# Kernel tuning notes

Hardware: AMD Instinct MI355X
Metric: run time of the kernel (lower is better)

The kernel has to match this reference:

```python
import jax, jax.numpy as jnp
import numpy as np

NUM_CLASSES = 8
SCORE_T = 0.5
IOU_T = 0.5
POSE_HYPS = 10
MAX_DET = 100
B, A = 1, 4096


def _pairwise_iou(bx):
    # bx: (N,4) in (x1,y1,x2,y2); TF-style +1 pixel convention
    x1 = jnp.maximum(bx[:, None, 0], bx[None, :, 0])
    y1 = jnp.maximum(bx[:, None, 1], bx[None, :, 1])
    x2 = jnp.minimum(bx[:, None, 2], bx[None, :, 2])
    y2 = jnp.minimum(bx[:, None, 3], bx[None, :, 3])
    wid = x2 - x1 + 1.0
    hei = y2 - y1 + 1.0
    inter = wid * hei
    area = (bx[:, 2] - bx[:, 0] + 1.0) * (bx[:, 3] - bx[:, 1] + 1.0)
    den = area[:, None] + area[None, :] - inter
    ov = jnp.where(den == 0.0, 0.0, inter / jnp.where(den == 0.0, 1.0, den))  # divide_no_nan
    return jnp.where((wid <= 0.0) | (hei <= 0.0), 0.0, ov)


def _per_class(scores_c, boxes_c, poses_c, conf_c):
    # Fixed-shape re-expression of _filter_detections: instead of compacting the
    # boxes with score > threshold (dynamic shape), keep all N and mask invalid
    # boxes out of the overlap indicator. Relative ordering (which drives the
    # argmax tie-break and the ascending sort) is identical to the compacted
    # subset, so the math matches exactly.
    N = scores_c.shape[0]
    K = POSE_HYPS + 1
    valid = scores_c > SCORE_T
    m = jnp.sum(valid.astype(jnp.int32))  # number of selected boxes
    ov = _pairwise_iou(boxes_c)  # (N,N)
    ind = ((ov > IOU_T) & valid[:, None] & valid[None, :]).astype(jnp.float32)
    # scatter_nd: true_ov[argmax_col(row i), i] = max(row i); column i is unique per update
    max_col = jnp.argmax(ind, axis=1)
    true_ov = jnp.zeros_like(ind).at[max_col, jnp.arange(N)].add(jnp.max(ind, axis=1))
    bc = (1.0 - ov) * true_ov * conf_c[None, :]
    bc = jnp.where(bc == 0.0, 1000.0, bc)  # 1000 = sentinel for 'not a hypothesis'
    # Only the first min(pose_hyps+1, m) ascending-sorted entries per row survive the
    # sequence mask, so take the K smallest instead of a full argsort (same result;
    # top_k of the negation breaks ties by lowest index like a stable ascending sort).
    neg, args = jax.lax.top_k(-bc, K)
    svals = -neg  # (N,K) K smallest per row
    hyp = (jnp.arange(K) < jnp.minimum(K, m)).astype(jnp.float32)
    cmask = jnp.where(svals == 1000.0, 0.0, 1.0) * hyp[None, :]
    denom = jnp.sum(cmask, axis=1)  # (N,)
    safe = jnp.where(denom == 0.0, 1.0, denom)
    poses_avg = jnp.where(denom[:, None] == 0.0, 0.0,
                          jnp.sum(cmask[:, :, None] * poses_c[args], axis=1) / safe[:, None])
    boxes_avg = jnp.where(denom[:, None] == 0.0, 0.0,
                          jnp.sum(cmask[:, :, None] * boxes_c[args], axis=1) / safe[:, None])
    return poses_avg, boxes_avg, denom > 0.0


def _forward(boxes3D, boxes, classification, poses, confidence):
    C = NUM_CLASSES
    N = classification.shape[0] * classification.shape[1]
    cls = classification.reshape(N, C)
    bxs = boxes.reshape(N, C, 4)
    pss = poses.reshape(N, C, 12)
    cnf = confidence.reshape(N, C)
    # boxes3D is reshaped/gathered by the original but never used afterwards (dead code)
    xs = (cls.T, jnp.transpose(bxs, (1, 0, 2)), jnp.transpose(pss, (1, 0, 2)), cnf.T)
    # serialize over classes so only one NxN working set is live at a time
    poses_avg, boxes_avg, survive = jax.lax.map(lambda t: _per_class(*t), xs)
    surv = survive.reshape(-1)  # (C*N,) class-major, matching the original concat order
    count = jnp.sum(surv.astype(jnp.int32))
    scores_flat = jnp.where(surv, cls.T.reshape(-1), -jnp.inf)
    top_scores, _ = jax.lax.top_k(scores_flat, MAX_DET)
    rank = jnp.arange(MAX_DET)
    ok = rank < count
    out_scores = jnp.where(ok, top_scores, -1.0)
    # NOTE: the original computes top_indices but never applies it — labels/poses/
    # indices/boxes stay in class-major survivor order, truncated/padded with -1.
    pos = jnp.arange(C * N)
    order = jnp.argsort(jnp.where(surv, pos, pos + C * N))  # stable compaction
    sel = order[:MAX_DET]
    labels_flat = jnp.repeat(jnp.arange(C), N)
    anchors_flat = jnp.tile(jnp.arange(N), C)
    out_labels = jnp.where(ok, labels_flat[sel], -1).astype(jnp.int32)
    out_idx = jnp.where(ok, anchors_flat[sel], -1).astype(jnp.int32)
    out_poses = jnp.where(ok[:, None], poses_avg.reshape(C * N, 12)[sel], -1.0)
    out_boxes = jnp.where(ok[:, None], boxes_avg.reshape(C * N, 4)[sel], -1.0)
    return out_scores, out_labels, out_poses, out_idx, out_boxes


def setup_inputs():
    key = jax.random.key(0)
    k1, k2, k3, k4, k5, k6 = jax.random.split(key, 6)
    C = NUM_CLASSES
    # realistic heavily-overlapping boxes in a 640x640 image
    cxy = jax.random.uniform(k1, (B, A, C, 2), minval=0.0, maxval=640.0)
    wh = jax.random.uniform(k2, (B, A, C, 2), minval=10.0, maxval=120.0)
    boxes = jnp.concatenate([cxy - wh / 2.0, cxy + wh / 2.0], axis=-1).reshape(B, A, C * 4)
    return {
        "boxes3D": jax.random.normal(k6, (B, A, C * 16), dtype=jnp.float32),
        "boxes": boxes,
        "classification": jax.random.uniform(k3, (B, A, C), dtype=jnp.float32),
        "poses": jax.random.normal(k4, (B, A, C * 12), dtype=jnp.float32),
        "confidence": jax.random.uniform(k5, (B, A, C), dtype=jnp.float32),
    }


def reference(boxes3D, boxes, classification, poses, confidence):
    return _forward(boxes3D, boxes, classification, poses, confidence)
```

## Files before the change

kernel.cpp:

```cpp
#include <hip/hip_runtime.h>
#include <stdint.h>

#define N_ANCH 4096
#define NCLS 8
#define CN (N_ANCH * NCLS)
#define SCORE_TH 0.5f
#define IOU_TH 0.5f
#define KSEL 11
#define MAX_DET 100
#define CAND_CAP 4096
#define TILE 128
#define TPC (N_ANCH / TILE)
#define NTRI (TPC * (TPC + 1) / 2)

__device__ __forceinline__ float iou_f(float4 a, float areaA, float4 b, float areaB) {
    float x1 = fmaxf(a.x, b.x);
    float y1 = fmaxf(a.y, b.y);
    float x2 = fminf(a.z, b.z);
    float y2 = fminf(a.w, b.w);
    float wid = x2 - x1 + 1.0f;
    float hei = y2 - y1 + 1.0f;
    float inter = wid * hei;
    float den = areaA + areaB - inter;
    float ov = (den == 0.0f) ? 0.0f : (inter / den);
    if (wid <= 0.0f || hei <= 0.0f) ov = 0.0f;
    return ov;
}

__global__ void __launch_bounds__(256) k_prep(const float* __restrict__ boxes,
                                              const float* __restrict__ cls,
                                              const float* __restrict__ conf,
                                              float4* boxesT, float* areaT,
                                              float* scoresT, float* confT,
                                              int* surv, int* minRank, int* hist) {
    int t = blockIdx.x * 256 + threadIdx.x;
    int n = t >> 3;
    int c = t & 7;
    int p = (c << 12) + n;
    scoresT[p] = cls[t];
    confT[p] = conf[t];
    float4 b = reinterpret_cast<const float4*>(boxes)[t];
    boxesT[p] = b;
    areaT[p] = (b.z - b.x + 1.0f) * (b.w - b.y + 1.0f);
    surv[t] = 0;
    minRank[t] = 0x7FFFFFFF;
    if (t < 1024) hist[t] = 0;
}

__global__ void __launch_bounds__(1024) k_validlist(const float* __restrict__ scoresT,
                                                    const float4* __restrict__ boxesT,
                                                    const float* __restrict__ areaT,
                                                    const float* __restrict__ confT,
                                                    int* validList, float4* vBox,
                                                    float* vArea, float* vConf, int* mVal) {
    int c = blockIdx.x;
    int tid = threadIdx.x;
    int lane = tid & 63, wid = tid >> 6;
    __shared__ int wsum[16];
    int cbase = c << 12;
    float4 sc = reinterpret_cast<const float4*>(scoresT + cbase)[tid];
    int f0 = sc.x > SCORE_TH, f1 = sc.y > SCORE_TH, f2 = sc.z > SCORE_TH, f3 = sc.w > SCORE_TH;
    int f = f0 + f1 + f2 + f3;
    int inc = f;
    for (int off = 1; off < 64; off <<= 1) {
        int o = __shfl_up(inc, off);
        if (lane >= off) inc += o;
    }
    if (lane == 63) wsum[wid] = inc;
    __syncthreads();
    int wbase = 0;
    for (int i = 0; i < wid; i++) wbase += wsum[i];
    int pos = wbase + inc - f;
    int n0 = tid * 4;
    int fl[4] = {f0, f1, f2, f3};
    #pragma unroll
    for (int d = 0; d < 4; d++) {
        if (fl[d]) {
            int n = n0 + d;
            validList[cbase + pos] = n;
            vBox[cbase + pos] = boxesT[cbase + n];
            vArea[cbase + pos] = areaT[cbase + n];
            vConf[cbase + pos] = confT[cbase + n];
            pos++;
        }
    }
    if (tid == 1023) mVal[c] = wbase + inc;
}

__global__ void __launch_bounds__(128) k_repmat(const float4* __restrict__ vBox,
                                                const float* __restrict__ vArea,
                                                const int* __restrict__ mVal,
                                                int* minRank) {
    int bid = blockIdx.x;
    int c = bid / NTRI;
    int t = bid - c * NTRI;
    int ci = (int)((sqrtf(8.0f * (float)t + 1.0f) - 1.0f) * 0.5f);
    while ((ci + 1) * (ci + 2) / 2 <= t) ci++;
    while (ci * (ci + 1) / 2 > t) ci--;
    int cj = t - ci * (ci + 1) / 2;
    int mc = mVal[c];
    int ib = ci * TILE, jb = cj * TILE;
    if (ib >= mc || jb >= mc) return;
    int tid = threadIdx.x;
    int cbase = c << 12;
    __shared__ float4 sB[TILE];
    __shared__ float sA[TILE];
    if (jb + tid < mc) {
        sB[tid] = vBox[cbase + jb + tid];
        sA[tid] = vArea[cbase + jb + tid];
    }
    __syncthreads();
    int i = ib + tid;
    if (i >= mc) return;
    float4 bk = vBox[cbase + i];
    float ak = vArea[cbase + i];
    int limit = min(TILE, mc - jb);
    if (ci == cj) limit = min(limit, i - jb);
    int lmin = 0x7FFFFFFF;
    #pragma unroll 4
    for (int r = 0; r < limit; r++) {
        float ov = iou_f(bk, ak, sB[r], sA[r]);
        if (ov > IOU_TH && r < lmin) lmin = r;
    }
    if (lmin != 0x7FFFFFFF) atomicMin(&minRank[cbase + i], jb + lmin);
}

__global__ void __launch_bounds__(256) k_repA(const float4* __restrict__ vBox,
                                              const float* __restrict__ vArea,
                                              const float* __restrict__ vConf,
                                              const int* __restrict__ validList,
                                              const int* __restrict__ mVal,
                                              const int* __restrict__ minRank,
                                              int* rep, int* surv) {
    int t = blockIdx.x * 256 + threadIdx.x;
    int c = t >> 12;
    int i = t & (N_ANCH - 1);
    int mc = mVal[c];
    if (i >= mc) return;
    int cbase = c << 12;
    int k = validList[cbase + i];
    int mr = minRank[cbase + i];
    if (mr > i) mr = i;
    int j = validList[cbase + mr];
    rep[cbase + k] = j;
    if (mr < i) {
        float ov = iou_f(vBox[cbase + i], vArea[cbase + i], vBox[cbase + mr], vArea[cbase + mr]);
        float bcv = (1.0f - ov) * vConf[cbase + i];
        if (bcv != 0.0f) surv[cbase + j] = 1;
    }
}

__global__ void __launch_bounds__(256) k_B(const int* __restrict__ surv,
                                           const float* __restrict__ scoresT,
                                           int* candPos, float* candScore,
                                           int* blockCnt, int* hist) {
    int bid = blockIdx.x, tid = threadIdx.x;
    int lane = tid & 63, w = tid >> 6;
    int t = bid * 256 + tid;
    int flag = surv[t] != 0;
    unsigned long long mask = __ballot(flag);
    __shared__ int wcnt[4];
    if (lane == 0) wcnt[w] = __popcll(mask);
    __syncthreads();
    int rank = __popcll(mask & ((1ull << lane) - 1ull));
    int wbase = 0;
    for (int i = 0; i < w; i++) wbase += wcnt[i];
    if (flag) {
        int local = wbase + rank;
        float v = scoresT[t];
        candPos[bid * 256 + local] = t;
        candScore[bid * 256 + local] = v;
        unsigned bits = __float_as_uint(v);
        int bb = (int)((bits - 0x3F000000u) >> 13);
        int bkt = bb < 0 ? 0 : (bb > 1023 ? 1023 : bb);
        atomicAdd(&hist[bkt], 1);
    }
    if (tid == 0) blockCnt[bid] = wcnt[0] + wcnt[1] + wcnt[2] + wcnt[3];
}

__global__ void __launch_bounds__(1024) k_C(const int* __restrict__ blockCnt,
                                            const int* __restrict__ hist,
                                            const int* __restrict__ candPos,
                                            const float* __restrict__ candScore,
                                            int* sel, int* count_g, float* out) {
    int tid = threadIdx.x;
    __shared__ int bc[128];
    __shared__ int offS[129];
    __shared__ int sfx[256];
    __shared__ int thrB;
    __shared__ int ccS;
    __shared__ float sc[CAND_CAP];
    if (tid < 128) bc[tid] = blockCnt[tid];
    if (tid == 0) { thrB = 0; ccS = 0; }
    __syncthreads();
    if (tid == 0) {
        int run = 0;
        for (int i = 0; i < 128; i++) { offS[i] = run; run += bc[i]; }
        offS[128] = run;
        *count_g = run;
    }
    __syncthreads();
    int count = offS[128];
    int target = count < MAX_DET ? count : MAX_DET;
    if (tid < target) {
        int lo = 0, hi = 127;
        while (lo < hi) { int mid = (lo + hi + 1) >> 1; if (offS[mid] <= tid) lo = mid; else hi = mid - 1; }
        sel[tid] = candPos[lo * 256 + (tid - offS[lo])];
    }
    if (tid < 256) {
        sfx[tid] = hist[4 * tid] + hist[4 * tid + 1] + hist[4 * tid + 2] + hist[4 * tid + 3];
    }
    __syncthreads();
    if (tid == 0) {
        int run = 0;
        for (int i = 255; i >= 0; i--) { int v = sfx[i]; sfx[i] = run; run += v; }
    }
    __syncthreads();
    if (tid < 256) {
        int S = sfx[tid];
        int found = -1;
        for (int b = 4 * tid + 3; b >= 4 * tid; b--) {
            S += hist[b];
            if (found < 0 && S >= target) found = b;
        }
        if (found >= 0) atomicMax(&thrB, found);
    }
    __syncthreads();
    int t0 = thrB;
    for (int pos = tid; pos < CN; pos += 1024) {
        int b = pos >> 8, l = pos & 255;
        if (l < bc[b]) {
            float v = candScore[pos];
            unsigned bits = __float_as_uint(v);
            int bb = (int)((bits - 0x3F000000u) >> 13);
            int bkt = bb < 0 ? 0 : (bb > 1023 ? 1023 : bb);
            if (bkt >= t0) {
                int id = atomicAdd(&ccS, 1);
                if (id < CAND_CAP) sc[id] = -v;
            }
        }
    }
    __syncthreads();
    int cc = ccS; if (cc > CAND_CAP) cc = CAND_CAP;
    int n = 128; while (n < cc) n <<= 1;
    for (int i = tid; i < n; i += 1024) if (i >= cc) sc[i] = 1e38f;
    __syncthreads();
    for (int kk = 2; kk <= n; kk <<= 1) {
        for (int jj = kk >> 1; jj > 0; jj >>= 1) {
            for (int i = tid; i < n; i += 1024) {
                int ixj = i ^ jj;
                if (ixj > i) {
                    float a = sc[i], b2 = sc[ixj];
                    bool up = ((i & kk) == 0);
                    if (up ? (a > b2) : (a < b2)) { sc[i] = b2; sc[ixj] = a; }
                }
            }
            __syncthreads();
        }
    }
    if (tid < MAX_DET) out[tid] = (tid < count) ? -sc[tid] : -1.0f;
}

__global__ void __launch_bounds__(256) k_out(const float4* __restrict__ boxesT,
                                             const float* __restrict__ areaT,
                                             const float* __restrict__ confT,
                                             const float* __restrict__ poses,
                                             const int* __restrict__ rep,
                                             const int* __restrict__ sel,
                                             const int* __restrict__ count_g,
                                             float* out) {
    int s = blockIdx.x;
    int tid = threadIdx.x;
    int lane = tid & 63, w = tid >> 6;
    int count = *count_g;
    if (s >= count) {
        if (tid == 0) { out[100 + s] = -1.0f; out[1400 + s] = -1.0f; }
        if (tid < 12) out[200 + s * 12 + tid] = -1.0f;
        if (tid >= 16 && tid < 20) out[1500 + s * 4 + (tid - 16)] = -1.0f;
        return;
    }
    int p = sel[s];
    int c = p >> 12;
    int r = p & (N_ANCH - 1);
    int cbase = c << 12;
    __shared__ unsigned long long keyArr[4096];
    __shared__ int nmS;
    __shared__ int kselS[KSEL];
    __shared__ unsigned long long bestS;
    __shared__ unsigned long long redK[4];
    if (tid == 0) nmS = 0;
    __syncthreads();
    float4 br = boxesT[cbase + r];
    float ar = areaT[cbase + r];
    for (int k = tid; k < N_ANCH; k += 256) {
        int rp = rep[cbase + k];
        if (rp == r && k != r) {
            float ov = iou_f(br, ar, boxesT[cbase + k], areaT[cbase + k]);
            float bcv = (1.0f - ov) * confT[cbase + k];
            if (bcv != 0.0f) {
                int id = atomicAdd(&nmS, 1);
                keyArr[id] = ((unsigned long long)__float_as_uint(bcv) << 32) | (unsigned)k;
            }
        }
    }
    __syncthreads();
    int nm = nmS;
    int dn = nm < KSEL ? nm : KSEL;
    if (nm > KSEL) {
        unsigned long long lastBest = ~0ull;
        for (int j = 0; j < KSEL; j++) {
            unsigned long long bk = ~0ull;
            for (int i = tid; i < nm; i += 256) {
                unsigned long long v = keyArr[i];
                if (v == lastBest) { keyArr[i] = ~0ull; v = ~0ull; }
                if (v < bk) bk = v;
            }
            for (int off = 32; off > 0; off >>= 1) {
                unsigned long long o = __shfl_down(bk, off);
                if (o < bk) bk = o;
            }
            if (lane == 0) redK[w] = bk;
            __syncthreads();
            if (tid == 0) {
                unsigned long long B = redK[0];
                for (int q2 = 1; q2 < 4; q2++) if (redK[q2] < B) B = redK[q2];
                bestS = B;
                kselS[j] = (int)(B & 0xFFFFFFFFull);
            }
            __syncthreads();
            lastBest = bestS;
        }
    } else if (tid < dn) {
        kselS[tid] = (int)(keyArr[tid] & 0xFFFFFFFFull);
    }
    __syncthreads();
    float fdn = (float)(dn > 0 ? dn : 1);
    if (tid < 12) {
        float ssum = 0.0f;
        for (int j = 0; j < dn; j++) ssum += poses[(kselS[j] * 8 + c) * 12 + tid];
        out[200 + s * 12 + tid] = ssum / fdn;
    } else if (tid < 16) {
        int d = tid - 12;
        float ssum = 0.0f;
        for (int j = 0; j < dn; j++) {
            const float* bb = (const float*)&boxesT[cbase + kselS[j]];
            ssum += bb[d];
        }
        out[1500 + s * 4 + d] = ssum / fdn;
    } else if (tid == 16) {
        out[100 + s] = (float)c;
    } else if (tid == 17) {
        out[1400 + s] = (float)r;
    }
}

extern "C" void kernel_launch(void* const* d_in, const int* in_sizes, int n_in,
                              void* d_out, int out_size, void* d_ws, size_t ws_size,
                              hipStream_t stream) {
    const float* boxes = (const float*)d_in[1];
    const float* cls   = (const float*)d_in[2];
    const float* poses = (const float*)d_in[3];
    const float* conf  = (const float*)d_in[4];
    float* out = (float*)d_out;

    char* ws = (char*)d_ws;
    size_t off = 0;
    auto alloc = [&](size_t bytes) {
        void* p = ws + off;
        off += (bytes + 255) & ~(size_t)255;
        return p;
    };
    float4* boxesT   = (float4*)alloc(CN * sizeof(float4));
    float*  areaT    = (float*)alloc(CN * sizeof(float));
    float*  scoresT  = (float*)alloc(CN * sizeof(float));
    float*  confT    = (float*)alloc(CN * sizeof(float));
    int*    validList= (int*)alloc(CN * sizeof(int));
    float4* vBox     = (float4*)alloc(CN * sizeof(float4));
    float*  vArea    = (float*)alloc(CN * sizeof(float));
    float*  vConf    = (float*)alloc(CN * sizeof(float));
    int*    mVal     = (int*)alloc(64);
    int*    rep      = (int*)alloc(CN * sizeof(int));
    int*    surv     = (int*)alloc(CN * sizeof(int));
    int*    minRank  = (int*)alloc(CN * sizeof(int));
    int*    sel      = (int*)alloc(MAX_DET * sizeof(int));
    int*    count_g  = (int*)alloc(64);
    int*    candPos  = (int*)alloc(CN * sizeof(int));
    float*  candScore= (float*)alloc(CN * sizeof(float));
    int*    hist     = (int*)alloc(1024 * sizeof(int));
    int*    blockCnt = (int*)alloc(128 * sizeof(int));

    k_prep<<<CN / 256, 256, 0, stream>>>(boxes, cls, conf, boxesT, areaT, scoresT, confT,
                                         surv, minRank, hist);
    k_validlist<<<NCLS, 1024, 0, stream>>>(scoresT, boxesT, areaT, confT,
                                           validList, vBox, vArea, vConf, mVal);
    k_repmat<<<NCLS * NTRI, 128, 0, stream>>>(vBox, vArea, mVal, minRank);
    k_repA<<<CN / 256, 256, 0, stream>>>(vBox, vArea, vConf, validList, mVal, minRank, rep, surv);
    k_B<<<CN / 256, 256, 0, stream>>>(surv, scoresT, candPos, candScore, blockCnt, hist);
    k_C<<<1, 1024, 0, stream>>>(blockCnt, hist, candPos, candScore, sel, count_g, out);
    k_out<<<MAX_DET, 256, 0, stream>>>(boxesT, areaT, confT, poses, rep, sel, count_g, out);
}
```

Before: 139.0 us.

## Fuse rep/survivor stages into repmat tail and merge selection with output

Folds the k_repA pass into k_repmat through a last-block-per-class pattern, using an atomic done counter so the final tile block of each class computes rep/surv and a per-class survivor count. k_B, k_C and k_out are merged into one k_final launch. Block 0 builds the histogram, picks the threshold and sorts the top scores, while the other blocks locate their detection by prefix-scanning surv and then do the hypothesis averaging with 1024 threads. This cuts the launch count from seven to four, and the intermediate candidate buffers are removed. In exchange, the tail of each class runs serially in a single 128-thread block, and block 0 scans all 32K entries by itself.

New measurement: 320.3 us. +130.3%, slower.

```diff
diff --git a/kernel.cpp b/kernel.cpp
--- a/kernel.cpp
+++ b/kernel.cpp
@@ -32,7 +32,7 @@
                                               const float* __restrict__ conf,
                                               float4* boxesT, float* areaT,
                                               float* scoresT, float* confT,
-                                              int* surv, int* minRank, int* hist) {
+                                              int* surv, int* minRank, int* done) {
     int t = blockIdx.x * 256 + threadIdx.x;
     int n = t >> 3;
     int c = t & 7;
@@ -44,7 +44,7 @@
     areaT[p] = (b.z - b.x + 1.0f) * (b.w - b.y + 1.0f);
     surv[t] = 0;
     minRank[t] = 0x7FFFFFFF;
-    if (t < 1024) hist[t] = 0;
+    if (t < 8) done[t] = 0;
 }
 
 __global__ void __launch_bounds__(1024) k_validlist(const float* __restrict__ scoresT,
@@ -89,8 +89,11 @@
 
 __global__ void __launch_bounds__(128) k_repmat(const float4* __restrict__ vBox,
                                                 const float* __restrict__ vArea,
+                                                const float* __restrict__ vConf,
+                                                const int* __restrict__ validList,
                                                 const int* __restrict__ mVal,
-                                                int* minRank) {
+                                                int* minRank, int* done,
+                                                int* rep, int* surv, int* classCnt) {
     int bid = blockIdx.x;
     int c = bid / NTRI;
     int t = bid - c * NTRI;
@@ -100,217 +103,222 @@
     int cj = t - ci * (ci + 1) / 2;
     int mc = mVal[c];
     int ib = ci * TILE, jb = cj * TILE;
-    if (ib >= mc || jb >= mc) return;
     int tid = threadIdx.x;
     int cbase = c << 12;
     __shared__ float4 sB[TILE];
     __shared__ float sA[TILE];
-    if (jb + tid < mc) {
-        sB[tid] = vBox[cbase + jb + tid];
-        sA[tid] = vArea[cbase + jb + tid];
-    }
-    __syncthreads();
-    int i = ib + tid;
-    if (i >= mc) return;
-    float4 bk = vBox[cbase + i];
-    float ak = vArea[cbase + i];
-    int limit = min(TILE, mc - jb);
-    if (ci == cj) limit = min(limit, i - jb);
-    int lmin = 0x7FFFFFFF;
-    #pragma unroll 4
-    for (int r = 0; r < limit; r++) {
-        float ov = iou_f(bk, ak, sB[r], sA[r]);
-        if (ov > IOU_TH && r < lmin) lmin = r;
-    }
-    if (lmin != 0x7FFFFFFF) atomicMin(&minRank[cbase + i], jb + lmin);
-}
-
-__global__ void __launch_bounds__(256) k_repA(const float4* __restrict__ vBox,
-                                              const float* __restrict__ vArea,
-                                              const float* __restrict__ vConf,
-                                              const int* __restrict__ validList,
-                                              const int* __restrict__ mVal,
-                                              const int* __restrict__ minRank,
-                                              int* rep, int* surv) {
-    int t = blockIdx.x * 256 + threadIdx.x;
-    int c = t >> 12;
-    int i = t & (N_ANCH - 1);
-    int mc = mVal[c];
-    if (i >= mc) return;
-    int cbase = c << 12;
-    int k = validList[cbase + i];
-    int mr = minRank[cbase + i];
-    if (mr > i) mr = i;
-    int j = validList[cbase + mr];
-    rep[cbase + k] = j;
-    if (mr < i) {
-        float ov = iou_f(vBox[cbase + i], vArea[cbase + i], vBox[cbase + mr], vArea[cbase + mr]);
-        float bcv = (1.0f - ov) * vConf[cbase + i];
-        if (bcv != 0.0f) surv[cbase + j] = 1;
-    }
-}
-
-__global__ void __launch_bounds__(256) k_B(const int* __restrict__ surv,
-                                           const float* __restrict__ scoresT,
-                                           int* candPos, float* candScore,
-                                           int* blockCnt, int* hist) {
+    __shared__ int lastS;
+    bool activeTile = (ib < mc) && (jb < mc);
+    if (activeTile) {
+        if (jb + tid < mc) {
+            sB[tid] = vBox[cbase + jb + tid];
+            sA[tid] = vArea[cbase + jb + tid];
+        }
+        __syncthreads();
+        int i = ib + tid;
+        if (i < mc) {
+            float4 bk = vBox[cbase + i];
+            float ak = vArea[cbase + i];
+            int limit = min(TILE, mc - jb);
+            if (ci == cj) limit = min(limit, i - jb);
+            int lmin = 0x7FFFFFFF;
+            #pragma unroll 4
+            for (int r = 0; r < limit; r++) {
+                float ov = iou_f(bk, ak, sB[r], sA[r]);
+                if (ov > IOU_TH && r < lmin) lmin = r;
+            }
+            if (lmin != 0x7FFFFFFF) atomicMin(&minRank[cbase + i], jb + lmin);
+        }
+    }
+    __syncthreads();
+    __threadfence();
+    if (tid == 0) {
+        int prev = __hip_atomic_fetch_add(&done[c], 1, __ATOMIC_ACQ_REL,
+                                          __HIP_MEMORY_SCOPE_AGENT);
+        lastS = (prev == NTRI - 1) ? 1 : 0;
+    }
+    __syncthreads();
+    if (!lastS) return;
+    __threadfence();
+    for (int i = tid; i < mc; i += 128) {
+        int k = validList[cbase + i];
+        int mr = __hip_atomic_load(&minRank[cbase + i], __ATOMIC_RELAXED,
+                                   __HIP_MEMORY_SCOPE_AGENT);
+        if (mr > i) mr = i;
+        int j = validList[cbase + mr];
+        rep[cbase + k] = j;
+        if (mr < i) {
+            float ov = iou_f(vBox[cbase + i], vArea[cbase + i],
+                             vBox[cbase + mr], vArea[cbase + mr]);
+            float bcv = (1.0f - ov) * vConf[cbase + i];
+            if (bcv != 0.0f) surv[cbase + j] = 1;
+        }
+    }
+    __syncthreads();
+    int cnt = 0;
+    for (int n = tid; n < N_ANCH; n += 128) cnt += (surv[cbase + n] != 0);
+    for (int off = 32; off > 0; off >>= 1) cnt += __shfl_down(cnt, off);
+    __shared__ int wred[2];
+    if ((tid & 63) == 0) wred[tid >> 6] = cnt;
+    __syncthreads();
+    if (tid == 0) classCnt[c] = wred[0] + wred[1];
+}
+
+__global__ void __launch_bounds__(1024) k_final(const float4* __restrict__ boxesT,
+                                                const float* __restrict__ areaT,
+                                                const float* __restrict__ confT,
+                                                const float* __restrict__ scoresT,
+                                                const float* __restrict__ poses,
+                                                const int* __restrict__ rep,
+                                                const int* __restrict__ surv,
+                                                const int* __restrict__ classCnt,
+                                                float* out) {
     int bid = blockIdx.x, tid = threadIdx.x;
     int lane = tid & 63, w = tid >> 6;
-    int t = bid * 256 + tid;
-    int flag = surv[t] != 0;
-    unsigned long long mask = __ballot(flag);
-    __shared__ int wcnt[4];
-    if (lane == 0) wcnt[w] = __popcll(mask);
-    __syncthreads();
-    int rank = __popcll(mask & ((1ull << lane) - 1ull));
-    int wbase = 0;
-    for (int i = 0; i < w; i++) wbase += wcnt[i];
-    if (flag) {
-        int local = wbase + rank;
-        float v = scoresT[t];
-        candPos[bid * 256 + local] = t;
-        candScore[bid * 256 + local] = v;
-        unsigned bits = __float_as_uint(v);
-        int bb = (int)((bits - 0x3F000000u) >> 13);
-        int bkt = bb < 0 ? 0 : (bb > 1023 ? 1023 : bb);
-        atomicAdd(&hist[bkt], 1);
-    }
-    if (tid == 0) blockCnt[bid] = wcnt[0] + wcnt[1] + wcnt[2] + wcnt[3];
-}
-
-__global__ void __launch_bounds__(1024) k_C(const int* __restrict__ blockCnt,
-                                            const int* __restrict__ hist,
-                                            const int* __restrict__ candPos,
-                                            const float* __restrict__ candScore,
-                                            int* sel, int* count_g, float* out) {
-    int tid = threadIdx.x;
-    __shared__ int bc[128];
-    __shared__ int offS[129];
+    __shared__ int coff[9];
+    __shared__ int hist[1024];
     __shared__ int sfx[256];
-    __shared__ int thrB;
-    __shared__ int ccS;
     __shared__ float sc[CAND_CAP];
-    if (tid < 128) bc[tid] = blockCnt[tid];
-    if (tid == 0) { thrB = 0; ccS = 0; }
-    __syncthreads();
-    if (tid == 0) {
-        int run = 0;
-        for (int i = 0; i < 128; i++) { offS[i] = run; run += bc[i]; }
-        offS[128] = run;
-        *count_g = run;
-    }
-    __syncthreads();
-    int count = offS[128];
-    int target = count < MAX_DET ? count : MAX_DET;
-    if (tid < target) {
-        int lo = 0, hi = 127;
-        while (lo < hi) { int mid = (lo + hi + 1) >> 1; if (offS[mid] <= tid) lo = mid; else hi = mid - 1; }
-        sel[tid] = candPos[lo * 256 + (tid - offS[lo])];
-    }
-    if (tid < 256) {
-        sfx[tid] = hist[4 * tid] + hist[4 * tid + 1] + hist[4 * tid + 2] + hist[4 * tid + 3];
-    }
-    __syncthreads();
-    if (tid == 0) {
-        int run = 0;
-        for (int i = 255; i >= 0; i--) { int v = sfx[i]; sfx[i] = run; run += v; }
-    }
-    __syncthreads();
-    if (tid < 256) {
-        int S = sfx[tid];
-        int found = -1;
-        for (int b = 4 * tid + 3; b >= 4 * tid; b--) {
-            S += hist[b];
-            if (found < 0 && S >= target) found = b;
-        }
-        if (found >= 0) atomicMax(&thrB, found);
-    }
-    __syncthreads();
-    int t0 = thrB;
-    for (int pos = tid; pos < CN; pos += 1024) {
-        int b = pos >> 8, l = pos & 255;
-        if (l < bc[b]) {
-            float v = candScore[pos];
-            unsigned bits = __float_as_uint(v);
-            int bb = (int)((bits - 0x3F000000u) >> 13);
-            int bkt = bb < 0 ? 0 : (bb > 1023 ? 1023 : bb);
-            if (bkt >= t0) {
-                int id = atomicAdd(&ccS, 1);
-                if (id < CAND_CAP) sc[id] = -v;
-            }
-        }
-    }
-    __syncthreads();
-    int cc = ccS; if (cc > CAND_CAP) cc = CAND_CAP;
-    int n = 128; while (n < cc) n <<= 1;
-    for (int i = tid; i < n; i += 1024) if (i >= cc) sc[i] = 1e38f;
-    __syncthreads();
-    for (int kk = 2; kk <= n; kk <<= 1) {
-        for (int jj = kk >> 1; jj > 0; jj >>= 1) {
-            for (int i = tid; i < n; i += 1024) {
-                int ixj = i ^ jj;
-                if (ixj > i) {
-                    float a = sc[i], b2 = sc[ixj];
-                    bool up = ((i & kk) == 0);
-                    if (up ? (a > b2) : (a < b2)) { sc[i] = b2; sc[ixj] = a; }
+    __shared__ unsigned long long keyArr[4096];
+    __shared__ int wsum[16];
+    __shared__ unsigned long long redK[16];
+    __shared__ int thrB, ccS, rS, nmS;
+    __shared__ unsigned long long bestS;
+
+    if (tid < 8) coff[tid + 1] = classCnt[tid];
+    if (tid == 0) coff[0] = 0;
+    __syncthreads();
+    if (tid == 0) for (int i = 0; i < 8; i++) coff[i + 1] += coff[i];
+    __syncthreads();
+    int count = coff[8];
+
+    if (bid == 0) {
+        hist[tid] = 0;
+        if (tid == 0) { thrB = 0; ccS = 0; }
+        __syncthreads();
+        for (int p = tid; p < CN; p += 1024) {
+            if (surv[p]) {
+                unsigned bits = __float_as_uint(scoresT[p]);
+                int bb = (int)((bits - 0x3F000000u) >> 13);
+                int bkt = bb < 0 ? 0 : (bb > 1023 ? 1023 : bb);
+                atomicAdd(&hist[bkt], 1);
+            }
+        }
+        __syncthreads();
+        int target = count < MAX_DET ? count : MAX_DET;
+        if (tid < 256)
+            sfx[tid] = hist[4 * tid] + hist[4 * tid + 1] + hist[4 * tid + 2] + hist[4 * tid + 3];
+        __syncthreads();
+        if (tid == 0) {
+            int run = 0;
+            for (int i = 255; i >= 0; i--) { int v = sfx[i]; sfx[i] = run; run += v; }
+        }
+        __syncthreads();
+        if (tid < 256) {
+            int S = sfx[tid];
+            int found = -1;
+            for (int b = 4 * tid + 3; b >= 4 * tid; b--) {
+                S += hist[b];
+                if (found < 0 && S >= target) found = b;
+            }
+            if (found >= 0) atomicMax(&thrB, found);
+        }
+        __syncthreads();
+        int t0 = thrB;
+        for (int p = tid; p < CN; p += 1024) {
+            if (surv[p]) {
+                float v = scoresT[p];
+                unsigned bits = __float_as_uint(v);
+                int bb = (int)((bits - 0x3F000000u) >> 13);
+                int bkt = bb < 0 ? 0 : (bb > 1023 ? 1023 : bb);
+                if (bkt >= t0) {
+                    int id = atomicAdd(&ccS, 1);
+                    if (id < CAND_CAP) sc[id] = -v;
                 }
             }
-            __syncthreads();
-        }
-    }
-    if (tid < MAX_DET) out[tid] = (tid < count) ? -sc[tid] : -1.0f;
-}
-
-__global__ void __launch_bounds__(256) k_out(const float4* __restrict__ boxesT,
-                                             const float* __restrict__ areaT,
-                                             const float* __restrict__ confT,
-                                             const float* __restrict__ poses,
-                                             const int* __restrict__ rep,
-                                             const int* __restrict__ sel,
-                                             const int* __restrict__ count_g,
-                                             float* out) {
-    int s = blockIdx.x;
-    int tid = threadIdx.x;
-    int lane = tid & 63, w = tid >> 6;
-    int count = *count_g;
+        }
+        __syncthreads();
+        int cc = ccS; if (cc > CAND_CAP) cc = CAND_CAP;
+        int n = 128; while (n < cc) n <<= 1;
+        for (int i = tid; i < n; i += 1024) if (i >= cc) sc[i] = 1e38f;
+        __syncthreads();
+        for (int kk = 2; kk <= n; kk <<= 1) {
+            for (int jj = kk >> 1; jj > 0; jj >>= 1) {
+                for (int i = tid; i < n; i += 1024) {
+                    int ixj = i ^ jj;
+                    if (ixj > i) {
+                        float a = sc[i], b2 = sc[ixj];
+                        bool up = ((i & kk) == 0);
+                        if (up ? (a > b2) : (a < b2)) { sc[i] = b2; sc[ixj] = a; }
+                    }
+                }
+                __syncthreads();
+            }
+        }
+        if (tid < MAX_DET) out[tid] = (tid < count) ? -sc[tid] : -1.0f;
+        return;
+    }
+
+    int s = bid - 1;
     if (s >= count) {
         if (tid == 0) { out[100 + s] = -1.0f; out[1400 + s] = -1.0f; }
         if (tid < 12) out[200 + s * 12 + tid] = -1.0f;
         if (tid >= 16 && tid < 20) out[1500 + s * 4 + (tid - 16)] = -1.0f;
         return;
     }
-    int p = sel[s];
-    int c = p >> 12;
-    int r = p & (N_ANCH - 1);
+    int c = 0;
+    while (coff[c + 1] <= s) c++;
+    int l = s - coff[c];
     int cbase = c << 12;
-    __shared__ unsigned long long keyArr[4096];
-    __shared__ int nmS;
-    __shared__ int kselS[KSEL];
-    __shared__ unsigned long long bestS;
-    __shared__ unsigned long long redK[4];
-    if (tid == 0) nmS = 0;
-    __syncthreads();
+    {
+        int4 sv = reinterpret_cast<const int4*>(surv + cbase)[tid];
+        int f0 = sv.x != 0, f1 = sv.y != 0, f2 = sv.z != 0, f3 = sv.w != 0;
+        int f = f0 + f1 + f2 + f3;
+        int inc = f;
+        for (int off = 1; off < 64; off <<= 1) {
+            int o = __shfl_up(inc, off);
+            if (lane >= off) inc += o;
+        }
+        if (lane == 63) wsum[w] = inc;
+        if (tid == 0) nmS = 0;
+        __syncthreads();
+        int base = 0;
+        for (int i = 0; i < w; i++) base += wsum[i];
+        int e = base + inc - f;
+        if (l >= e && l < e + f) {
+            int need = l - e;
+            int fl[4] = {f0, f1, f2, f3};
+            #pragma unroll
+            for (int d = 0; d < 4; d++) {
+                if (fl[d]) { if (need == 0) rS = 4 * tid + d; need--; }
+            }
+        }
+        __syncthreads();
+    }
+    int r = rS;
     float4 br = boxesT[cbase + r];
     float ar = areaT[cbase + r];
-    for (int k = tid; k < N_ANCH; k += 256) {
+    for (int k = tid; k < N_ANCH; k += 1024) {
         int rp = rep[cbase + k];
         if (rp == r && k != r) {
             float ov = iou_f(br, ar, boxesT[cbase + k], areaT[cbase + k]);
             float bcv = (1.0f - ov) * confT[cbase + k];
             if (bcv != 0.0f) {
                 int id = atomicAdd(&nmS, 1);
-                keyArr[id] = ((unsigned long long)__float_as_uint(bcv) << 32) | (unsigned)k;
+                if (id < 4096)
+                    keyArr[id] = ((unsigned long long)__float_as_uint(bcv) << 32) | (unsigned)k;
             }
         }
     }
     __syncthreads();
     int nm = nmS;
     int dn = nm < KSEL ? nm : KSEL;
+    __shared__ int kselS[KSEL];
     if (nm > KSEL) {
         unsigned long long lastBest = ~0ull;
         for (int j = 0; j < KSEL; j++) {
             unsigned long long bk = ~0ull;
-            for (int i = tid; i < nm; i += 256) {
+            for (int i = tid; i < nm; i += 1024) {
                 unsigned long long v = keyArr[i];
                 if (v == lastBest) { keyArr[i] = ~0ull; v = ~0ull; }
                 if (v < bk) bk = v;
@@ -323,7 +331,7 @@
             __syncthreads();
             if (tid == 0) {
                 unsigned long long B = redK[0];
-                for (int q2 = 1; q2 < 4; q2++) if (redK[q2] < B) B = redK[q2];
+                for (int q2 = 1; q2 < 16; q2++) if (redK[q2] < B) B = redK[q2];
                 bestS = B;
                 kselS[j] = (int)(B & 0xFFFFFFFFull);
             }
@@ -382,20 +390,15 @@
     int*    rep      = (int*)alloc(CN * sizeof(int));
     int*    surv     = (int*)alloc(CN * sizeof(int));
     int*    minRank  = (int*)alloc(CN * sizeof(int));
-    int*    sel      = (int*)alloc(MAX_DET * sizeof(int));
-    int*    count_g  = (int*)alloc(64);
-    int*    candPos  = (int*)alloc(CN * sizeof(int));
-    float*  candScore= (float*)alloc(CN * sizeof(float));
-    int*    hist     = (int*)alloc(1024 * sizeof(int));
-    int*    blockCnt = (int*)alloc(128 * sizeof(int));
+    int*    done     = (int*)alloc(64);
+    int*    classCnt = (int*)alloc(64);
 
     k_prep<<<CN / 256, 256, 0, stream>>>(boxes, cls, conf, boxesT, areaT, scoresT, confT,
-                                         surv, minRank, hist);
+                                         surv, minRank, done);
     k_validlist<<<NCLS, 1024, 0, stream>>>(scoresT, boxesT, areaT, confT,
                                            validList, vBox, vArea, vConf, mVal);
-    k_repmat<<<NCLS * NTRI, 128, 0, stream>>>(vBox, vArea, mVal, minRank);
-    k_repA<<<CN / 256, 256, 0, stream>>>(vBox, vArea, vConf, validList, mVal, minRank, rep, surv);
-    k_B<<<CN / 256, 256, 0, stream>>>(surv, scoresT, candPos, candScore, blockCnt, hist);
-    k_C<<<1, 1024, 0, stream>>>(blockCnt, hist, candPos, candScore, sel, count_g, out);
-    k_out<<<MAX_DET, 256, 0, stream>>>(boxesT, areaT, confT, poses, rep, sel, count_g, out);
-}
+    k_repmat<<<NCLS * NTRI, 128, 0, stream>>>(vBox, vArea, vConf, validList, mVal,
+                                              minRank, done, rep, surv, classCnt);
+    k_final<<<1 + MAX_DET, 1024, 0, stream>>>(boxesT, areaT, confT, scoresT, poses,
+                                              rep, surv, classCnt, out);
+}
```
